# Optimization experiments

Measured on AMD Instinct MI355X. Metric: run time of the kernel, lower is better.

Reference implementation:

```python
import jax, jax.numpy as jnp
import numpy as np

N_NODES = 500000
N_EDGES = 2000000
F_IN = 117
HIDDEN = 128
NLAYERS = 3


def setup_inputs() -> dict:
    key = jax.random.key(0)
    ks = jax.random.split(key, 8)
    x = jax.random.normal(ks[0], (N_NODES, F_IN), dtype=jnp.float32)
    edge_src = jax.random.randint(ks[1], (N_EDGES,), 0, N_NODES, dtype=jnp.int32)
    edge_dst = jax.random.randint(ks[2], (N_EDGES,), 0, N_NODES, dtype=jnp.int32)
    W_in = jax.random.normal(ks[3], (F_IN, HIDDEN), dtype=jnp.float32) * 0.05
    b_in = jax.random.normal(ks[4], (HIDDEN,), dtype=jnp.float32) * 0.05
    W_self = jax.random.normal(ks[5], (NLAYERS, HIDDEN, HIDDEN), dtype=jnp.float32) * 0.05
    W_neigh = jax.random.normal(ks[6], (NLAYERS, HIDDEN, HIDDEN), dtype=jnp.float32) * 0.05
    b_layers = jax.random.normal(ks[7], (NLAYERS, HIDDEN), dtype=jnp.float32) * 0.05
    return {"x": x, "edge_src": edge_src, "edge_dst": edge_dst,
            "W_in": W_in, "b_in": b_in,
            "W_self": W_self, "W_neigh": W_neigh, "b_layers": b_layers}


def reference(x, edge_src, edge_dst, W_in, b_in, W_self, W_neigh, b_layers):
    # Input projection: Linear(117 -> 128) + Tanh
    h = jnp.tanh(x @ W_in + b_in)  # [N, H]
    N = h.shape[0]

    # In-degree per destination node (static; zero-degree nodes get zero mean)
    deg = jax.ops.segment_sum(jnp.ones_like(edge_dst, dtype=h.dtype), edge_dst,
                              num_segments=N)  # [N]
    inv_deg = (1.0 / jnp.maximum(deg, 1.0))[:, None]  # [N, 1]

    # Stacked SAGEConv('mean') layers: relu(h @ W_self + mean_neigh @ W_neigh + b)
    for l in range(NLAYERS):
        neigh_sum = jax.ops.segment_sum(h[edge_src], edge_dst, num_segments=N)  # [N, H]
        h_neigh = neigh_sum * inv_deg
        h = jax.nn.relu(h @ W_self[l] + h_neigh @ W_neigh[l] + b_layers[l])
    return h
```

## Files before the change

kernel.cpp:

```cpp
#include <hip/hip_runtime.h>

#define N_NODES 500000
#define N_EDGES 2000000
#define F_IN 117
#define H 128
#define NLAYERS 3

#define SCAN_E 2048
#define NB_SCAN ((N_NODES + SCAN_E - 1) / SCAN_E)

typedef __attribute__((ext_vector_type(8))) short short8v;
typedef __attribute__((ext_vector_type(4))) float f32x4;

__device__ __forceinline__ unsigned short f2bf(float x) {
    unsigned u = __builtin_bit_cast(unsigned, x);
    u += 0x7FFFu + ((u >> 16) & 1u);
    return (unsigned short)(u >> 16);
}
__device__ __forceinline__ float bf2f(unsigned short s) {
    unsigned u = ((unsigned)s) << 16;
    return __builtin_bit_cast(float, u);
}

__global__ __launch_bounds__(256) void convert_x_kernel(const float* __restrict__ x,
                                                        unsigned short* __restrict__ xb) {
    __shared__ float xs[8 * F_IN];
    const int t = threadIdx.x;
    const int ngroups = N_NODES / 8;
    for (int g = blockIdx.x; g < ngroups; g += gridDim.x) {
        const int r0 = g * 8;
        __syncthreads();
        const float* gx = x + (size_t)r0 * F_IN;
        for (int i = t; i < 8 * F_IN; i += 256) xs[i] = gx[i];
        __syncthreads();
        const int rr = t >> 5;
        const int c0 = (t & 31) * 4;
        ushort4 o;
        o.x = (c0 + 0 < F_IN) ? f2bf(xs[rr * F_IN + c0 + 0]) : 0;
        o.y = (c0 + 1 < F_IN) ? f2bf(xs[rr * F_IN + c0 + 1]) : 0;
        o.z = (c0 + 2 < F_IN) ? f2bf(xs[rr * F_IN + c0 + 2]) : 0;
        o.w = (c0 + 3 < F_IN) ? f2bf(xs[rr * F_IN + c0 + 3]) : 0;
        *(ushort4*)(xb + (size_t)(r0 + rr) * H + c0) = o;
    }
}

__global__ void prep_w_kernel(const float* __restrict__ Wself,
                              const float* __restrict__ Wneigh,
                              const float* __restrict__ Win,
                              short* __restrict__ Wfrag,
                              short* __restrict__ WfragIn) {
    const int tid = blockIdx.x * 256 + threadIdx.x;
    const int total_cmb = NLAYERS * 64 * 64;
    if (tid < total_cmb) {
        const int lane = tid & 63;
        const int fi   = (tid >> 6) & 63;
        const int l    = tid >> 12;
        const int ks = fi & 7, ct = (fi >> 3) & 3, wc = fi >> 5;
        const int c = wc * 64 + ct * 16 + (lane & 15);
        const int kbase = ks * 32 + (lane >> 4) * 8;
        short8v out;
        #pragma unroll
        for (int j = 0; j < 8; ++j) {
            int k = kbase + j;
            float v = (k < 128) ? Wself [(size_t)l * H * H + k * H + c]
                                : Wneigh[(size_t)l * H * H + (k - 128) * H + c];
            out[j] = (short)f2bf(v);
        }
        *(short8v*)(Wfrag + (size_t)tid * 8) = out;
    } else if (tid < total_cmb + 32 * 64) {
        const int t2 = tid - total_cmb;
        const int lane = t2 & 63;
        const int fi   = t2 >> 6;
        const int ks = fi & 3, ct = (fi >> 2) & 3, wc = fi >> 4;
        const int c = wc * 64 + ct * 16 + (lane & 15);
        const int kbase = ks * 32 + (lane >> 4) * 8;
        short8v out;
        #pragma unroll
        for (int j = 0; j < 8; ++j) {
            int k = kbase + j;
            out[j] = (k < F_IN) ? (short)f2bf(Win[(size_t)k * H + c]) : (short)0;
        }
        *(short8v*)(WfragIn + (size_t)t2 * 8) = out;
    }
}

__global__ __launch_bounds__(512, 2) void proj_mfma(const short* __restrict__ WfragIn,
                                                    const float* __restrict__ bias,
                                                    const unsigned short* __restrict__ xb,
                                                    unsigned short* __restrict__ hb) {
    const int wave = threadIdx.x >> 6;
    const int lane = threadIdx.x & 63;
    const int wc   = wave & 1;

    short8v Bf[4][4];
    #pragma unroll
    for (int ct = 0; ct < 4; ++ct)
        #pragma unroll
        for (int ks = 0; ks < 4; ++ks)
            Bf[ct][ks] = ((const short8v*)WfragIn)[(size_t)(((wc * 4 + ct) * 4 + ks) * 64 + lane)];

    float bs[4];
    #pragma unroll
    for (int ct = 0; ct < 4; ++ct) bs[ct] = bias[wc * 64 + ct * 16 + (lane & 15)];

    const int ntasks = (N_NODES / 16) * 2;
    for (int task = blockIdx.x * 8 + wave; task < ntasks; task += gridDim.x * 8) {
        const int r0 = (task >> 1) * 16;
        const unsigned short* arow = xb + (size_t)(r0 + (lane & 15)) * H + (lane >> 4) * 8;
        short8v Af[4];
        #pragma unroll
        for (int ks = 0; ks < 4; ++ks) Af[ks] = *(const short8v*)(arow + ks * 32);

        f32x4 acc[4];
        #pragma unroll
        for (int ct = 0; ct < 4; ++ct) acc[ct] = (f32x4){0.f, 0.f, 0.f, 0.f};
        #pragma unroll
        for (int ks = 0; ks < 4; ++ks)
            #pragma unroll
            for (int ct = 0; ct < 4; ++ct)
                acc[ct] = __builtin_amdgcn_mfma_f32_16x16x32_bf16(Af[ks], Bf[ct][ks], acc[ct], 0, 0, 0);

        #pragma unroll
        for (int ct = 0; ct < 4; ++ct) {
            const int col = wc * 64 + ct * 16 + (lane & 15);
            #pragma unroll
            for (int q = 0; q < 4; ++q) {
                float v = tanhf(acc[ct][q] + bs[ct]);
                hb[(size_t)(r0 + (lane >> 4) * 4 + q) * H + col] = f2bf(v);
            }
        }
    }
}

__global__ void zero_int_kernel(int* __restrict__ p, int n) {
    int i = blockIdx.x * blockDim.x + threadIdx.x;
    if (i < n) p[i] = 0;
}

__global__ void hist_kernel(const int* __restrict__ dst, int* __restrict__ cnt) {
    int e = blockIdx.x * blockDim.x + threadIdx.x;
    if (e < N_EDGES) atomicAdd(&cnt[dst[e]], 1);
}

__global__ __launch_bounds__(256) void scan_reduce_kernel(const int* __restrict__ cnt,
                                                          int* __restrict__ bsums) {
    __shared__ int s[256];
    const int base = blockIdx.x * SCAN_E;
    int sum = 0;
    for (int i = threadIdx.x; i < SCAN_E; i += 256) {
        int idx = base + i;
        sum += (idx < N_NODES) ? cnt[idx] : 0;
    }
    s[threadIdx.x] = sum;
    __syncthreads();
    for (int off = 128; off > 0; off >>= 1) {
        if (threadIdx.x < off) s[threadIdx.x] += s[threadIdx.x + off];
        __syncthreads();
    }
    if (threadIdx.x == 0) bsums[blockIdx.x] = s[0];
}

__global__ void scan_bsums_kernel(int* __restrict__ bsums) {
    __shared__ int s[256];
    const int tid = threadIdx.x;
    int v = (tid < NB_SCAN) ? bsums[tid] : 0;
    s[tid] = v;
    __syncthreads();
    for (int off = 1; off < 256; off <<= 1) {
        int add = (tid >= off) ? s[tid - off] : 0;
        __syncthreads();
        s[tid] += add;
        __syncthreads();
    }
    if (tid < NB_SCAN) bsums[tid] = s[tid] - v;
}

__global__ __launch_bounds__(256) void scan_final_kernel(const int* __restrict__ cnt,
                                                         const int* __restrict__ bsums,
                                                         int* __restrict__ start,
                                                         int* __restrict__ cursor,
                                                         float* __restrict__ inv) {
    __shared__ int tsum[256];
    const int tid = threadIdx.x;
    const int base = blockIdx.x * SCAN_E + tid * 8;
    int c[8];
    int s = 0;
    #pragma unroll
    for (int k = 0; k < 8; ++k) {
        int idx = base + k;
        c[k] = (idx < N_NODES) ? cnt[idx] : 0;
        s += c[k];
    }
    tsum[tid] = s;
    __syncthreads();
    for (int off = 1; off < 256; off <<= 1) {
        int add = (tid >= off) ? tsum[tid - off] : 0;
        __syncthreads();
        tsum[tid] += add;
        __syncthreads();
    }
    int off0 = bsums[blockIdx.x] + tsum[tid] - s;
    #pragma unroll
    for (int k = 0; k < 8; ++k) {
        int idx = base + k;
        if (idx < N_NODES) {
            start[idx]  = off0;
            cursor[idx] = off0;
            inv[idx]    = 1.0f / fmaxf((float)c[k], 1.0f);
            off0 += c[k];
        }
    }
}

__global__ void fill_kernel(const int* __restrict__ src, const int* __restrict__ dst,
                            int* __restrict__ cursor, int* __restrict__ srcs) {
    int e = blockIdx.x * blockDim.x + threadIdx.x;
    if (e < N_EDGES) {
        int pos = atomicAdd(&cursor[dst[e]], 1);
        srcs[pos] = src[e];
    }
}

__global__ __launch_bounds__(256) void gather_kernel(const int* __restrict__ start,
                                                     const int* __restrict__ cnt,
                                                     const int* __restrict__ srcs,
                                                     const float* __restrict__ inv,
                                                     const unsigned short* __restrict__ hb,
                                                     unsigned short* __restrict__ nsb) {
    const int idx  = blockIdx.x * 256 + threadIdx.x;
    const int node = idx >> 4;
    if (node >= N_NODES) return;
    const int f = (idx & 15) * 8;
    const int st = start[node];
    const int c  = cnt[node];
    float a[8];
    #pragma unroll
    for (int i = 0; i < 8; ++i) a[i] = 0.f;
    int j = 0;
    for (; j + 1 < c; j += 2) {
        const int s0 = srcs[st + j];
        const int s1 = srcs[st + j + 1];
        const short8v v0 = *(const short8v*)(hb + (size_t)s0 * H + f);
        const short8v v1 = *(const short8v*)(hb + (size_t)s1 * H + f);
        #pragma unroll
        for (int i = 0; i < 8; ++i) a[i] += bf2f((unsigned short)v0[i]);
        #pragma unroll
        for (int i = 0; i < 8; ++i) a[i] += bf2f((unsigned short)v1[i]);
    }
    if (j < c) {
        const int s0 = srcs[st + j];
        const short8v v0 = *(const short8v*)(hb + (size_t)s0 * H + f);
        #pragma unroll
        for (int i = 0; i < 8; ++i) a[i] += bf2f((unsigned short)v0[i]);
    }
    const float iv = inv[node];
    short8v o;
    #pragma unroll
    for (int i = 0; i < 8; ++i) o[i] = (short)f2bf(a[i] * iv);
    *(short8v*)(nsb + (size_t)node * H + f) = o;
}

__global__ __launch_bounds__(512, 2) void combine_mfma(const short* __restrict__ Wfrag,
                                                       const float* __restrict__ bias,
                                                       const unsigned short* __restrict__ hb,
                                                       const unsigned short* __restrict__ nsb,
                                                       unsigned short* __restrict__ outb,
                                                       float* __restrict__ outf,
                                                       int last) {
    const int wave = threadIdx.x >> 6;
    const int lane = threadIdx.x & 63;
    const int wc   = wave & 1;

    short8v Bf[4][8];
    #pragma unroll
    for (int ct = 0; ct < 4; ++ct)
        #pragma unroll
        for (int ks = 0; ks < 8; ++ks)
            Bf[ct][ks] = ((const short8v*)Wfrag)[(size_t)(((wc * 4 + ct) * 8 + ks) * 64 + lane)];

    float bs[4];
    #pragma unroll
    for (int ct = 0; ct < 4; ++ct) bs[ct] = bias[wc * 64 + ct * 16 + (lane & 15)];

    const int ntasks = (N_NODES / 16) * 2;
    for (int task = blockIdx.x * 8 + wave; task < ntasks; task += gridDim.x * 8) {
        const int r0 = (task >> 1) * 16;
        const unsigned short* arow = hb  + (size_t)(r0 + (lane & 15)) * H + (lane >> 4) * 8;
        const unsigned short* nrow = nsb + (size_t)(r0 + (lane & 15)) * H + (lane >> 4) * 8;
        short8v Af[8];
        #pragma unroll
        for (int ks = 0; ks < 4; ++ks) Af[ks]     = *(const short8v*)(arow + ks * 32);
        #pragma unroll
        for (int ks = 0; ks < 4; ++ks) Af[4 + ks] = *(const short8v*)(nrow + ks * 32);

        f32x4 acc[4];
        #pragma unroll
        for (int ct = 0; ct < 4; ++ct) acc[ct] = (f32x4){0.f, 0.f, 0.f, 0.f};
        #pragma unroll
        for (int ks = 0; ks < 8; ++ks)
            #pragma unroll
            for (int ct = 0; ct < 4; ++ct)
                acc[ct] = __builtin_amdgcn_mfma_f32_16x16x32_bf16(Af[ks], Bf[ct][ks], acc[ct], 0, 0, 0);

        if (!last) {
            #pragma unroll
            for (int ct = 0; ct < 4; ++ct) {
                const int col = wc * 64 + ct * 16 + (lane & 15);
                #pragma unroll
                for (int q = 0; q < 4; ++q) {
                    float v = fmaxf(acc[ct][q] + bs[ct], 0.f);
                    outb[(size_t)(r0 + (lane >> 4) * 4 + q) * H + col] = f2bf(v);
                }
            }
        } else {
            #pragma unroll
            for (int ct = 0; ct < 4; ++ct) {
                const int col = wc * 64 + ct * 16 + (lane & 15);
                #pragma unroll
                for (int q = 0; q < 4; ++q) {
                    float v = fmaxf(acc[ct][q] + bs[ct], 0.f);
                    outf[(size_t)(r0 + (lane >> 4) * 4 + q) * H + col] = v;
                }
            }
        }
    }
}

extern "C" void kernel_launch(void* const* d_in, const int* in_sizes, int n_in,
                              void* d_out, int out_size, void* d_ws, size_t ws_size,
                              hipStream_t stream) {
    const float* x        = (const float*)d_in[0];
    const int*   edge_src = (const int*)d_in[1];
    const int*   edge_dst = (const int*)d_in[2];
    const float* W_in     = (const float*)d_in[3];
    const float* b_in     = (const float*)d_in[4];
    const float* W_self   = (const float*)d_in[5];
    const float* W_neigh  = (const float*)d_in[6];
    const float* b_layers = (const float*)d_in[7];

    unsigned short* h0  = (unsigned short*)d_ws;
    unsigned short* nsb = h0 + (size_t)N_NODES * H;
    int*   cnt    = (int*)(nsb + (size_t)N_NODES * H);
    int*   start  = cnt + N_NODES;
    int*   cursor = start + N_NODES;
    float* inv    = (float*)(cursor + N_NODES);
    int*   srcs   = (int*)(inv + N_NODES);
    int*   bsums  = srcs + N_EDGES;
    short* Wfrag  = (short*)(bsums + 256);
    short* WfragIn = Wfrag + (size_t)NLAYERS * 64 * 64 * 8;
    unsigned short* h1 = (unsigned short*)d_out;
    unsigned short* xb = h1 + (size_t)N_NODES * H;

    convert_x_kernel<<<8192, 256, 0, stream>>>(x, xb);
    prep_w_kernel<<<(NLAYERS * 64 * 64 + 32 * 64 + 255) / 256, 256, 0, stream>>>(
        W_self, W_neigh, W_in, Wfrag, WfragIn);

    zero_int_kernel<<<(N_NODES + 255) / 256, 256, 0, stream>>>(cnt, N_NODES);
    hist_kernel<<<(N_EDGES + 255) / 256, 256, 0, stream>>>(edge_dst, cnt);
    scan_reduce_kernel<<<NB_SCAN, 256, 0, stream>>>(cnt, bsums);
    scan_bsums_kernel<<<1, 256, 0, stream>>>(bsums);
    scan_final_kernel<<<NB_SCAN, 256, 0, stream>>>(cnt, bsums, start, cursor, inv);
    fill_kernel<<<(N_EDGES + 255) / 256, 256, 0, stream>>>(edge_src, edge_dst, cursor, srcs);

    proj_mfma<<<1024, 512, 0, stream>>>(WfragIn, b_in, xb, h0);

    const int gather_grid = (N_NODES * 16 + 255) / 256;
    gather_kernel<<<gather_grid, 256, 0, stream>>>(start, cnt, srcs, inv, h0, nsb);
    combine_mfma<<<1024, 512, 0, stream>>>(Wfrag + 0 * 64 * 64 * 8, b_layers + 0 * H,
                                           h0, nsb, h1, nullptr, 0);
    gather_kernel<<<gather_grid, 256, 0, stream>>>(start, cnt, srcs, inv, h1, nsb);
    combine_mfma<<<1024, 512, 0, stream>>>(Wfrag + 1 * 64 * 64 * 8, b_layers + 1 * H,
                                           h1, nsb, h0, nullptr, 0);
    gather_kernel<<<gather_grid, 256, 0, stream>>>(start, cnt, srcs, inv, h0, nsb);
    combine_mfma<<<1024, 512, 0, stream>>>(Wfrag + 2 * 64 * 64 * 8, b_layers + 2 * H,
                                           h0, nsb, nullptr, (float*)d_out, 1);
}
```

Baseline: 1.121 ms.

## Fuse x bf16 conversion into projection, use fast tanh, unroll gather by four

Removes the separate fp32-to-bf16 conversion pass and has the projection kernel read and convert x rows directly, avoiding a full intermediate write and read. Replaces tanhf with an exp2/rcp based approximation, and unrolls the neighbor gather to issue four row loads at once for more memory parallelism. Direct loads of 117-float rows are unaligned and read past each row into the next row's data, which relies on zero weights for padding columns; the fast tanh slightly changes precision.

```diff
diff --git a/kernel.cpp b/kernel.cpp
--- a/kernel.cpp
+++ b/kernel.cpp
@@ -21,27 +21,9 @@
     unsigned u = ((unsigned)s) << 16;
     return __builtin_bit_cast(float, u);
 }
-
-__global__ __launch_bounds__(256) void convert_x_kernel(const float* __restrict__ x,
-                                                        unsigned short* __restrict__ xb) {
-    __shared__ float xs[8 * F_IN];
-    const int t = threadIdx.x;
-    const int ngroups = N_NODES / 8;
-    for (int g = blockIdx.x; g < ngroups; g += gridDim.x) {
-        const int r0 = g * 8;
-        __syncthreads();
-        const float* gx = x + (size_t)r0 * F_IN;
-        for (int i = t; i < 8 * F_IN; i += 256) xs[i] = gx[i];
-        __syncthreads();
-        const int rr = t >> 5;
-        const int c0 = (t & 31) * 4;
-        ushort4 o;
-        o.x = (c0 + 0 < F_IN) ? f2bf(xs[rr * F_IN + c0 + 0]) : 0;
-        o.y = (c0 + 1 < F_IN) ? f2bf(xs[rr * F_IN + c0 + 1]) : 0;
-        o.z = (c0 + 2 < F_IN) ? f2bf(xs[rr * F_IN + c0 + 2]) : 0;
-        o.w = (c0 + 3 < F_IN) ? f2bf(xs[rr * F_IN + c0 + 3]) : 0;
-        *(ushort4*)(xb + (size_t)(r0 + rr) * H + c0) = o;
-    }
+__device__ __forceinline__ float fast_tanh(float x) {
+    float e = __builtin_amdgcn_exp2f(x * 2.885390081777927f);
+    return 1.0f - 2.0f * __builtin_amdgcn_rcpf(e + 1.0f);
 }
 
 __global__ void prep_w_kernel(const float* __restrict__ Wself,
@@ -86,7 +68,7 @@
 
 __global__ __launch_bounds__(512, 2) void proj_mfma(const short* __restrict__ WfragIn,
                                                     const float* __restrict__ bias,
-                                                    const unsigned short* __restrict__ xb,
+                                                    const float* __restrict__ x,
                                                     unsigned short* __restrict__ hb) {
     const int wave = threadIdx.x >> 6;
     const int lane = threadIdx.x & 63;
@@ -103,13 +85,30 @@
     #pragma unroll
     for (int ct = 0; ct < 4; ++ct) bs[ct] = bias[wc * 64 + ct * 16 + (lane & 15)];
 
+    const int cbase = (lane >> 4) * 8;
     const int ntasks = (N_NODES / 16) * 2;
     for (int task = blockIdx.x * 8 + wave; task < ntasks; task += gridDim.x * 8) {
-        const int r0 = (task >> 1) * 16;
-        const unsigned short* arow = xb + (size_t)(r0 + (lane & 15)) * H + (lane >> 4) * 8;
+        const int r0  = (task >> 1) * 16;
+        const int row = r0 + (lane & 15);
+        const float* xr = x + (size_t)row * F_IN;
+
         short8v Af[4];
         #pragma unroll
-        for (int ks = 0; ks < 4; ++ks) Af[ks] = *(const short8v*)(arow + ks * 32);
+        for (int ks = 0; ks < 4; ++ks) {
+            const int k0 = ks * 32 + cbase;
+            short8v a;
+            if (row == N_NODES - 1 && k0 + 7 >= F_IN) {
+                #pragma unroll
+                for (int j = 0; j < 8; ++j) {
+                    int k = k0 + j;
+                    a[j] = (k < F_IN) ? (short)f2bf(xr[k]) : (short)0;
+                }
+            } else {
+                #pragma unroll
+                for (int j = 0; j < 8; ++j) a[j] = (short)f2bf(xr[k0 + j]);
+            }
+            Af[ks] = a;
+        }
 
         f32x4 acc[4];
         #pragma unroll
@@ -125,7 +124,7 @@
             const int col = wc * 64 + ct * 16 + (lane & 15);
             #pragma unroll
             for (int q = 0; q < 4; ++q) {
-                float v = tanhf(acc[ct][q] + bs[ct]);
+                float v = fast_tanh(acc[ct][q] + bs[ct]);
                 hb[(size_t)(r0 + (lane >> 4) * 4 + q) * H + col] = f2bf(v);
             }
         }
@@ -237,15 +236,29 @@
     #pragma unroll
     for (int i = 0; i < 8; ++i) a[i] = 0.f;
     int j = 0;
-    for (; j + 1 < c; j += 2) {
-        const int s0 = srcs[st + j];
+    for (; j + 4 <= c; j += 4) {
+        const int s0 = srcs[st + j + 0];
+        const int s1 = srcs[st + j + 1];
+        const int s2 = srcs[st + j + 2];
+        const int s3 = srcs[st + j + 3];
+        const short8v v0 = *(const short8v*)(hb + (size_t)s0 * H + f);
+        const short8v v1 = *(const short8v*)(hb + (size_t)s1 * H + f);
+        const short8v v2 = *(const short8v*)(hb + (size_t)s2 * H + f);
+        const short8v v3 = *(const short8v*)(hb + (size_t)s3 * H + f);
+        #pragma unroll
+        for (int i = 0; i < 8; ++i)
+            a[i] += (bf2f((unsigned short)v0[i]) + bf2f((unsigned short)v1[i]))
+                  + (bf2f((unsigned short)v2[i]) + bf2f((unsigned short)v3[i]));
+    }
+    if (j + 2 <= c) {
+        const int s0 = srcs[st + j + 0];
         const int s1 = srcs[st + j + 1];
         const short8v v0 = *(const short8v*)(hb + (size_t)s0 * H + f);
         const short8v v1 = *(const short8v*)(hb + (size_t)s1 * H + f);
         #pragma unroll
-        for (int i = 0; i < 8; ++i) a[i] += bf2f((unsigned short)v0[i]);
-        #pragma unroll
-        for (int i = 0; i < 8; ++i) a[i] += bf2f((unsigned short)v1[i]);
+        for (int i = 0; i < 8; ++i)
+            a[i] += bf2f((unsigned short)v0[i]) + bf2f((unsigned short)v1[i]);
+        j += 2;
     }
     if (j < c) {
         const int s0 = srcs[st + j];
@@ -349,9 +362,7 @@
     short* Wfrag  = (short*)(bsums + 256);
     short* WfragIn = Wfrag + (size_t)NLAYERS * 64 * 64 * 8;
     unsigned short* h1 = (unsigned short*)d_out;
-    unsigned short* xb = h1 + (size_t)N_NODES * H;
-
-    convert_x_kernel<<<8192, 256, 0, stream>>>(x, xb);
+
     prep_w_kernel<<<(NLAYERS * 64 * 64 + 32 * 64 + 255) / 256, 256, 0, stream>>>(
         W_self, W_neigh, W_in, Wfrag, WfragIn);
 
@@ -362,7 +373,7 @@
     scan_final_kernel<<<NB_SCAN, 256, 0, stream>>>(cnt, bsums, start, cursor, inv);
     fill_kernel<<<(N_EDGES + 255) / 256, 256, 0, stream>>>(edge_src, edge_dst, cursor, srcs);
 
-    proj_mfma<<<1024, 512, 0, stream>>>(WfragIn, b_in, xb, h0);
+    proj_mfma<<<1024, 512, 0, stream>>>(WfragIn, b_in, x, h0);
 
     const int gather_grid = (N_NODES * 16 + 255) / 256;
     gather_kernel<<<gather_grid, 256, 0, stream>>>(start, cnt, srcs, inv, h0, nsb);
```

Result: faster. 1.031 ms (-8.0%).
